# Optimization experiments

Hardware: AMD Instinct MI355X
Metric: run time of the kernel (lower is better)

The kernel has to match this reference:

```python
import jax, jax.numpy as jnp
import numpy as np
from jax import lax

N_NODES = 5000; N_EDGES = 160000; N_FEAT = 128; HIDDEN = 256
N_TPL = 10; N_TPL_NODES = 10; N_CLASSES = 8
ALPHA = 0.5          # FGW structure/feature trade-off
CG_ITERS = 5         # conditional-gradient (Frank-Wolfe) outer iterations
SINK_ITERS = 30      # log-domain Sinkhorn iterations (EMD surrogate)
SINK_REG = 0.02      # entropic reg relative to cost scale


def setup_inputs() -> dict:
    key = jax.random.key(0)
    ks = jax.random.split(key, 8)
    x = jax.random.normal(ks[0], (N_NODES, N_FEAT), jnp.float32)
    edge_index = jax.random.randint(ks[1], (2, N_EDGES), 0, N_NODES)
    W1 = jax.random.normal(ks[2], (N_FEAT, HIDDEN), jnp.float32) / np.sqrt(N_FEAT)
    b1 = jnp.zeros((HIDDEN,), jnp.float32)
    W2 = jax.random.normal(ks[3], (HIDDEN, N_FEAT), jnp.float32) / np.sqrt(HIDDEN)
    b2 = jnp.zeros((N_FEAT,), jnp.float32)
    templates = jax.random.uniform(ks[4], (N_TPL, N_TPL_NODES, N_TPL_NODES), jnp.float32)
    templates_features = jax.random.uniform(ks[5], (N_TPL, N_TPL_NODES, N_FEAT), jnp.float32)
    Wlin = jax.random.normal(ks[6], (N_TPL, N_CLASSES), jnp.float32) / np.sqrt(N_TPL)
    blin = jnp.zeros((N_CLASSES,), jnp.float32)
    return dict(x=x, edge_index=edge_index, W1=W1, b1=b1, W2=W2, b2=b2,
                templates=templates, templates_features=templates_features,
                Wlin=Wlin, blin=blin)


def gcn_conv(x, src, dst, W, b):
    # PyG GCNConv: x @ W, then D^-1/2 (A + I) D^-1/2 aggregation, then + b
    n = x.shape[0]
    loop = jnp.arange(n)
    s = jnp.concatenate([src, loop]); d = jnp.concatenate([dst, loop])
    deg = jax.ops.segment_sum(jnp.ones(s.shape[0], x.dtype), d, num_segments=n)
    dinv = lax.rsqrt(jnp.maximum(deg, 1.0))
    h = x @ W
    msg = h[s] * (dinv[s] * dinv[d])[:, None]
    return jax.ops.segment_sum(msg, d, num_segments=n) + b


def sinkhorn_log(G, logp, logq):
    # entropic OT in log domain as a jit-friendly surrogate for exact EMD
    scale = lax.stop_gradient(jnp.max(jnp.abs(G)) + 1e-9)
    mlogK = -G / (SINK_REG * scale)          # [n, m]
    f0 = jnp.zeros(G.shape[0], G.dtype); g0 = jnp.zeros(G.shape[1], G.dtype)
    def body(carry, _):
        f, g = carry
        g = logq - jax.nn.logsumexp(mlogK + f[:, None], axis=0)
        f = logp - jax.nn.logsumexp(mlogK + g[None, :], axis=1)
        return (f, g), None
    (f, g), _ = lax.scan(body, (f0, g0), None, length=SINK_ITERS)
    return jnp.exp(f[:, None] + mlogK + g[None, :])


def fgw2(C1, x, C2, F2):
    # Fused Gromov-Wasserstein distance (square loss), uniform weights,
    # conditional-gradient with fixed step 2/(t+2) and Sinkhorn LP surrogate.
    n, m = C1.shape[0], C2.shape[0]
    p = jnp.full((n,), 1.0 / n, x.dtype); q = jnp.full((m,), 1.0 / m, x.dtype)
    logp = jnp.log(p); logq = jnp.log(q)
    # squared-euclidean feature cost  [n, m]
    M = jnp.sum(x * x, 1)[:, None] + jnp.sum(F2 * F2, 1)[None, :] - 2.0 * x @ F2.T
    # square-loss GW decomposition: f1=a^2, f2=b^2, h1=a, h2=2b
    constC = ((C1 * C1) @ p)[:, None] + ((C2 * C2) @ q)[None, :]
    def tens(T):
        return constC - C1 @ T @ (2.0 * C2).T
    T = p[:, None] * q[None, :]
    for t in range(CG_ITERS):
        grad = (1.0 - ALPHA) * M + 2.0 * ALPHA * tens(T)
        Tnew = sinkhorn_log(grad, logp, logq)
        T = T + (2.0 / (t + 2.0)) * (Tnew - T)
    return (1.0 - ALPHA) * jnp.sum(M * T) + ALPHA * jnp.sum(tens(T) * T)


def reference(x, edge_index, W1, b1, W2, b2, templates, templates_features, Wlin, blin):
    src, dst = edge_index[0], edge_index[1]
    h = jax.nn.relu(gcn_conv(x, src, dst, W1, b1))
    h = gcn_conv(h, src, dst, W2, b2)           # [N, F]
    n = x.shape[0]
    C = jnp.zeros((n, n), x.dtype).at[src, dst].set(1.0)   # dense adjacency
    dists = jax.vmap(lambda Ct, Ft: fgw2(C, h, Ct, Ft))(templates, templates_features)  # [K]
    return dists @ Wlin + blin                  # [num_classes]
```

## Files before the change

kernel.cpp:

```cpp
#include <hip/hip_runtime.h>
#include <cstdint>

#define NND 5000
#define NE 160000
#define NF 128
#define NH 256
#define NT 10
#define MT 10
#define NC 8
#define NMAT (NND*MT)
#define CG_ITERS 5
#define SINK_IT 30

#if __has_builtin(__builtin_amdgcn_update_dpp)
#define DPP_ADD(x, ctrl, rmask) \
    ((x) + __int_as_float(__builtin_amdgcn_update_dpp(0, __float_as_int(x), (ctrl), (rmask), 0xf, true)))
__device__ __forceinline__ float wave_sum63(float x) {
    x = DPP_ADD(x, 0x111, 0xf);
    x = DPP_ADD(x, 0x112, 0xf);
    x = DPP_ADD(x, 0x114, 0xf);
    x = DPP_ADD(x, 0x118, 0xf);
    x = DPP_ADD(x, 0x142, 0xa);
    x = DPP_ADD(x, 0x143, 0xc);
    return x;
}
#else
__device__ __forceinline__ float wave_sum63(float x) {
#pragma unroll
    for (int off = 32; off; off >>= 1) x += __shfl_xor(x, off);
    return x;
}
#endif

__device__ __forceinline__ float frcp(float x) {
#if __has_builtin(__builtin_amdgcn_rcpf)
    return __builtin_amdgcn_rcpf(x);
#else
    return 1.f / x;
#endif
}


__global__ void k_edge1(const int* __restrict__ src, const int* __restrict__ dst,
                        int* __restrict__ cntD, unsigned* __restrict__ bitmap,
                        int* __restrict__ cntS, unsigned char* __restrict__ keep) {
    for (int e = blockIdx.x*blockDim.x + threadIdx.x; e < NE; e += gridDim.x*blockDim.x) {
        int s = src[e], d = dst[e];
        atomicAdd(&cntD[d], 1);
        int key = s * NND + d;
        unsigned bit = 1u << (key & 31);
        unsigned old = atomicOr(&bitmap[key >> 5], bit);
        if (!(old & bit)) { keep[e] = 1; atomicAdd(&cntS[s], 1); }
        else keep[e] = 0;
    }
}

__global__ void k_exscan2(const int* __restrict__ cntD, int* __restrict__ rpD,
                          float* __restrict__ dinv,
                          const int* __restrict__ cntS, int* __restrict__ rpS,
                          float* __restrict__ c1row,
                          const float* __restrict__ tpl, float* __restrict__ c2row) {
    const int T = 1024;
    int tid = threadIdx.x;
    if (blockIdx.x == 2) {
        if (tid < NT * MT) {
            int t = tid / MT, j = tid % MT;
            float s = 0.f;
            for (int k = 0; k < MT; k++) { float v = tpl[t * 100 + j * 10 + k]; s += v * v; }
            c2row[tid] = s * (1.f / MT);
        }
        return;
    }
    const int* cnt = blockIdx.x ? cntS : cntD;
    int* rp = blockIdx.x ? rpS : rpD;
    int C = (NND + T - 1) / T;
    int begin = tid * C, end = begin + C; if (end > NND) end = NND; if (begin > NND) begin = NND;
    int s = 0;
    for (int i = begin; i < end; i++) s += cnt[i];
    __shared__ int part[1024];
    part[tid] = s; __syncthreads();
    for (int off = 1; off < T; off <<= 1) {
        int v = (tid >= off) ? part[tid - off] : 0;
        __syncthreads();
        part[tid] += v;
        __syncthreads();
    }
    int run = part[tid] - s;
    for (int i = begin; i < end; i++) { rp[i] = run; run += cnt[i]; }
    if (tid == T - 1) rp[NND] = part[T - 1];
    if (blockIdx.x == 0)
        for (int i = begin; i < end; i++) dinv[i] = rsqrtf((float)(cnt[i] + 1));
    else
        for (int i = begin; i < end; i++) c1row[i] = (float)cnt[i] * (1.f / NND);
}

__global__ void k_scatter2(const int* __restrict__ src, const int* __restrict__ dst,
                           const unsigned char* __restrict__ keep,
                           const int* __restrict__ rpD, int* __restrict__ cur1,
                           int* __restrict__ csrS, float* __restrict__ csrC,
                           const float* __restrict__ dinv,
                           const int* __restrict__ rpS, int* __restrict__ cur2,
                           int* __restrict__ csrD) {
    for (int e = blockIdx.x*blockDim.x + threadIdx.x; e < NE; e += gridDim.x*blockDim.x) {
        int s = src[e], d = dst[e];
        int pos = rpD[d] + atomicAdd(&cur1[d], 1);
        csrS[pos] = s;
        csrC[pos] = dinv[s] * dinv[d];
        if (keep[e]) {
            int p2 = rpS[s] + atomicAdd(&cur2[s], 1);
            csrD[p2] = d;
        }
    }
}


__global__ __launch_bounds__(256) void k_gemm(const float* __restrict__ A,
                                              const float* __restrict__ B,
                                              float* __restrict__ C, int M, int N, int K,
                                              const float* __restrict__ bias, int relu) {
    const int BM = 64, BN = 64, BK = 16;
    __shared__ float As[BK][BM + 1];
    __shared__ float Bs[BK][BN];
    int tid = threadIdx.x;
    int row0 = blockIdx.y * BM, col0 = blockIdx.x * BN;
    int tx = tid % 16, ty = tid / 16;
    float acc[4][4] = {};
    for (int k0 = 0; k0 < K; k0 += BK) {
#pragma unroll
        for (int l = 0; l < 4; l++) {
            int idx = tid + l * 256;
            int r = idx / BK, kk = idx % BK;
            int gr = row0 + r;
            As[kk][r] = (gr < M) ? A[(size_t)gr * K + k0 + kk] : 0.f;
        }
#pragma unroll
        for (int l = 0; l < 4; l++) {
            int idx = tid + l * 256;
            int kk = idx / BN, c = idx % BN;
            Bs[kk][c] = B[(size_t)(k0 + kk) * N + col0 + c];
        }
        __syncthreads();
#pragma unroll
        for (int kk = 0; kk < BK; kk++) {
            float a[4], b[4];
#pragma unroll
            for (int i = 0; i < 4; i++) a[i] = As[kk][ty * 4 + i];
#pragma unroll
            for (int j = 0; j < 4; j++) b[j] = Bs[kk][tx * 4 + j];
#pragma unroll
            for (int i = 0; i < 4; i++)
#pragma unroll
                for (int j = 0; j < 4; j++) acc[i][j] += a[i] * b[j];
        }
        __syncthreads();
    }
#pragma unroll
    for (int i = 0; i < 4; i++) {
        int gr = row0 + ty * 4 + i;
        if (gr < M) {
#pragma unroll
            for (int j = 0; j < 4; j++) {
                int gc = col0 + tx * 4 + j;
                float o = acc[i][j];
                if (bias) o += bias[gc];
                if (relu) o = fmaxf(o, 0.f);
                C[(size_t)gr * N + gc] = o;
            }
        }
    }
}

__global__ __launch_bounds__(256) void k_aggregate(const float4* __restrict__ hin4,
                            const float* __restrict__ bias,
                            float4* __restrict__ hout4, const int* __restrict__ rp,
                            const int* __restrict__ csrS, const float* __restrict__ csrC,
                            const float* __restrict__ dinv) {
    int v = blockIdx.x * 8 + (threadIdx.x >> 5);
    int l = threadIdx.x & 31;
    float dv = dinv[v];
    float sc = dv * dv;
    float4 a = hin4[(size_t)v * 32 + l];
    float4 acc = make_float4(a.x * sc, a.y * sc, a.z * sc, a.w * sc);
    int e0 = rp[v], e1 = rp[v + 1];
    for (int e = e0; e < e1; e++) {
        int s = csrS[e];
        float c = csrC[e];
        float4 hv = hin4[(size_t)s * 32 + l];
        acc.x = fmaf(hv.x, c, acc.x);
        acc.y = fmaf(hv.y, c, acc.y);
        acc.z = fmaf(hv.z, c, acc.z);
        acc.w = fmaf(hv.w, c, acc.w);
    }
    if (bias) {
        float4 bb = ((const float4*)bias)[l];
        acc.x += bb.x; acc.y += bb.y; acc.z += bb.z; acc.w += bb.w;
    }
    hout4[(size_t)v * 32 + l] = acc;
}


__global__ __launch_bounds__(128) void k_M(const float* __restrict__ h,
                    const float* __restrict__ tplF,
                    float* __restrict__ Mout, float* __restrict__ T) {
    int i = blockIdx.x;
    int tid = threadIdx.x;
    int lane = tid & 63, w = tid >> 6;
    __shared__ float hrow[NF];
    __shared__ float part[2];
    float hv = h[(size_t)i * NF + tid];
    hrow[tid] = hv;
    float ps = wave_sum63(hv * hv);
    if (lane == 63) part[w] = ps;
    __syncthreads();
    float sx = part[0] + part[1];
    int c = tid;
    if (c < NT * MT) {
        const float4* Fc = (const float4*)(tplF + (size_t)c * NF);
        const float4* hr = (const float4*)hrow;
        float dot = 0.f, nrm = 0.f;
#pragma unroll 8
        for (int f = 0; f < NF / 4; f++) {
            float4 fv = Fc[f];
            float4 hq = hr[f];
            dot = fmaf(hq.x, fv.x, dot); dot = fmaf(hq.y, fv.y, dot);
            dot = fmaf(hq.z, fv.z, dot); dot = fmaf(hq.w, fv.w, dot);
            nrm = fmaf(fv.x, fv.x, nrm); nrm = fmaf(fv.y, fv.y, nrm);
            nrm = fmaf(fv.z, fv.z, nrm); nrm = fmaf(fv.w, fv.w, nrm);
        }
        int t = c / MT, j = c % MT;
        Mout[(size_t)t * NMAT + (size_t)i * MT + j] = sx + nrm - 2.f * dot;
        T[(size_t)t * NMAT + (size_t)i * MT + j] = 1.f / (float)NMAT;
    }
}


__global__ __launch_bounds__(256) void k_grad(const float* __restrict__ T, const float* __restrict__ Mm,
                                              const float* __restrict__ c1row, const float* __restrict__ c2row,
                                              const float* __restrict__ tpl,
                                              const int* __restrict__ rpS, const int* __restrict__ csrD,
                                              float* __restrict__ G, unsigned* __restrict__ scaleBits) {
    int t = blockIdx.y;
    int tid = threadIdx.x;
    __shared__ float tC2[100];
    if (tid < 100) tC2[tid] = 2.f * tpl[t * 100 + tid];
    __syncthreads();
    int i = blockIdx.x * 256 + tid;
    float amax = 0.f;
    if (i < NND) {
        const float* Tt = T + (size_t)t * NMAT;
        const float* Mt = Mm + (size_t)t * NMAT;
        float* Gt = G + (size_t)t * NMAT;
        float L[MT];
#pragma unroll
        for (int j = 0; j < MT; j++) L[j] = 0.f;
        int e0 = rpS[i], e1 = rpS[i + 1];
        for (int e = e0; e < e1; e++) {
            int k = csrD[e];
            const float* Tk = Tt + (size_t)k * MT;
#pragma unroll
            for (int j = 0; j < MT; j++) L[j] += Tk[j];
        }
        float c1 = c1row[i];
#pragma unroll
        for (int j = 0; j < MT; j++) {
            float s = 0.f;
#pragma unroll
            for (int k = 0; k < MT; k++) s += L[k] * tC2[j * 10 + k];
            float g = 0.5f * Mt[(size_t)i * MT + j] + (c1 + c2row[t * 10 + j] - s);
            Gt[(size_t)i * MT + j] = g;
            amax = fmaxf(amax, fabsf(g));
        }
    }
    __shared__ float red[256];
    red[tid] = amax; __syncthreads();
    for (int off = 128; off > 0; off >>= 1) {
        if (tid < off) red[tid] = fmaxf(red[tid], red[tid + off]);
        __syncthreads();
    }
    if (tid == 0) atomicMax(&scaleBits[t], __float_as_uint(red[0]));
}

__global__ __attribute__((amdgpu_flat_work_group_size(512, 512), amdgpu_waves_per_eu(2, 2)))
void k_sinkhorn(const float* __restrict__ G,
                const unsigned* __restrict__ scaleBits,
                float* __restrict__ T, float step) {
    int t = blockIdx.x;
    int tid = threadIdx.x;
    int lane = tid & 63, w = tid >> 6;
    float sc = __uint_as_float(scaleBits[t]) + 1e-9f;
    float inv = -1.f / (0.02f * sc);
    const float* Gt = G + (size_t)t * NMAT;
    float* Tt = T + (size_t)t * NMAT;

    __shared__ float wred[8][10];
    __shared__ float4 vbc4[3];

    float Kf[10][10];
    float u[10];
#pragma unroll
    for (int r = 0; r < 10; r++) {
        int i = tid + r * 512;
        if (i < NND) {
            u[r] = 1.f;
            const float2* Gr = (const float2*)(Gt + (size_t)i * 10);
#pragma unroll
            for (int h = 0; h < 5; h++) {
                float2 g = Gr[h];
                Kf[r][2*h]   = __expf(g.x * inv);
                Kf[r][2*h+1] = __expf(g.y * inv);
            }
        } else {
            u[r] = 0.f;
#pragma unroll
            for (int j = 0; j < 10; j++) Kf[r][j] = 0.f;
        }
    }

    float vv[10];

    for (int it = 0; it < SINK_IT; it++) {
        float S[10];
#pragma unroll
        for (int j = 0; j < 10; j++) S[j] = 0.f;
#pragma unroll
        for (int r = 0; r < 10; r++) {
            float ur = u[r];
#pragma unroll
            for (int j = 0; j < 10; j++) S[j] = fmaf(Kf[r][j], ur, S[j]);
        }
#pragma unroll
        for (int j = 0; j < 10; j++) {
            float s = wave_sum63(S[j]);
            if (lane == 63) wred[w][j] = s;
        }
        __syncthreads();
        if (tid < 10) {
            float s = 0.f;
#pragma unroll
            for (int q = 0; q < 8; q++) s += wred[q][tid];
            ((float*)vbc4)[tid] = 0.1f * frcp(fmaxf(s, 1e-30f));
        }
        __syncthreads();
        {
            float4 a = vbc4[0], b = vbc4[1], c = vbc4[2];
            vv[0]=a.x; vv[1]=a.y; vv[2]=a.z; vv[3]=a.w;
            vv[4]=b.x; vv[5]=b.y; vv[6]=b.z; vv[7]=b.w;
            vv[8]=c.x; vv[9]=c.y;
        }
#pragma unroll
        for (int r = 0; r < 10; r++) {
            float R = 0.f;
#pragma unroll
            for (int j = 0; j < 10; j++) R = fmaf(Kf[r][j], vv[j], R);
            u[r] = (tid + r * 512 < NND) ? (2e-4f * frcp(fmaxf(R, 1e-30f))) : 0.f;
        }
    }

#pragma unroll
    for (int r = 0; r < 10; r++) {
        int i = tid + r * 512;
        if (i < NND) {
            float ur = u[r];
            float2* Tr = (float2*)(Tt + (size_t)i * 10);
#pragma unroll
            for (int h = 0; h < 5; h++) {
                float2 v = Tr[h];
                v.x += step * (ur * Kf[r][2*h]   * vv[2*h]   - v.x);
                v.y += step * (ur * Kf[r][2*h+1] * vv[2*h+1] - v.y);
                Tr[h] = v;
            }
        }
    }
}


__global__ __launch_bounds__(256) void k_final(const float* __restrict__ T, const float* __restrict__ Mm,
                                               const float* __restrict__ c1row, const float* __restrict__ c2row,
                                               const float* __restrict__ tpl,
                                               const int* __restrict__ rpS, const int* __restrict__ csrD,
                                               double* __restrict__ dd, int* __restrict__ done,
                                               const float* __restrict__ Wlin,
                                               const float* __restrict__ blin,
                                               float* __restrict__ out) {
    int t = blockIdx.y;
    int tid = threadIdx.x;
    __shared__ float tC2[100];
    if (tid < 100) tC2[tid] = 2.f * tpl[t * 100 + tid];
    __syncthreads();
    int i = blockIdx.x * 256 + tid;
    double msum = 0.0, tsum = 0.0;
    if (i < NND) {
        const float* Tt = T + (size_t)t * NMAT;
        const float* Mt = Mm + (size_t)t * NMAT;
        float L[MT];
#pragma unroll
        for (int j = 0; j < MT; j++) L[j] = 0.f;
        int e0 = rpS[i], e1 = rpS[i + 1];
        for (int e = e0; e < e1; e++) {
            int k = csrD[e];
            const float* Tk = Tt + (size_t)k * MT;
#pragma unroll
            for (int j = 0; j < MT; j++) L[j] += Tk[j];
        }
        float c1 = c1row[i];
#pragma unroll
        for (int j = 0; j < MT; j++) {
            float s = 0.f;
#pragma unroll
            for (int k = 0; k < MT; k++) s += L[k] * tC2[j * 10 + k];
            float ts = c1 + c2row[t * 10 + j] - s;
            float Tv = Tt[(size_t)i * MT + j];
            msum += (double)(Mt[(size_t)i * MT + j] * Tv);
            tsum += (double)(ts * Tv);
        }
    }
    __shared__ double r1[256], r2[256];
    r1[tid] = msum; r2[tid] = tsum; __syncthreads();
    for (int off = 128; off > 0; off >>= 1) {
        if (tid < off) { r1[tid] += r1[tid + off]; r2[tid] += r2[tid + off]; }
        __syncthreads();
    }
    if (tid == 0) {
        atomicAdd(&dd[t * 2], r1[0]);
        atomicAdd(&dd[t * 2 + 1], r2[0]);
        __threadfence();
        int prev = atomicAdd(done, 1);
        if (prev == 20 * NT - 1) {
            __threadfence();
            float ds[NT];
#pragma unroll
            for (int k = 0; k < NT; k++) {
                unsigned long long b0 = __hip_atomic_load((unsigned long long*)&dd[2*k],
                                        __ATOMIC_RELAXED, __HIP_MEMORY_SCOPE_AGENT);
                unsigned long long b1 = __hip_atomic_load((unsigned long long*)&dd[2*k+1],
                                        __ATOMIC_RELAXED, __HIP_MEMORY_SCOPE_AGENT);
                ds[k] = 0.5f * (float)(__longlong_as_double(b0) + __longlong_as_double(b1));
            }
#pragma unroll
            for (int c = 0; c < NC; c++) {
                float o = blin[c];
#pragma unroll
                for (int k = 0; k < NT; k++) o = fmaf(ds[k], Wlin[k * NC + c], o);
                out[c] = o;
            }
        }
    }
}


extern "C" void kernel_launch(void* const* d_in, const int* in_sizes, int n_in,
                              void* d_out, int out_size, void* d_ws, size_t ws_size,
                              hipStream_t stream) {
    const float* x    = (const float*)d_in[0];
    const int*   ei   = (const int*)d_in[1];
    const int*   src  = ei;
    const int*   dst  = ei + NE;
    const float* W1   = (const float*)d_in[2];
    const float* b1   = (const float*)d_in[3];
    const float* W2   = (const float*)d_in[4];
    const float* b2   = (const float*)d_in[5];
    const float* tpl  = (const float*)d_in[6];
    const float* tplF = (const float*)d_in[7];
    const float* Wlin = (const float*)d_in[8];
    const float* blin = (const float*)d_in[9];
    float* out = (float*)d_out;

    char* w = (char*)d_ws;
    size_t off = 0;
    auto alloc = [&](size_t b) -> char* {
        off = (off + 255) & ~(size_t)255;
        char* p = w + off; off += b; return p;
    };
    float* bufA = (float*)alloc((size_t)NND * NH * 4);
    float* bufB = (float*)alloc((size_t)NND * NH * 4);
    float* bufH = (float*)alloc((size_t)NND * NF * 4);
    float* Mm   = (float*)alloc((size_t)NT * NMAT * 4);
    float* T    = (float*)alloc((size_t)NT * NMAT * 4);
    float* G    = (float*)alloc((size_t)NT * NMAT * 4);
    int* cntD = (int*)alloc((size_t)NND * 4);
    int* cntS = (int*)alloc((size_t)NND * 4);
    int* cur1 = (int*)alloc((size_t)NND * 4);
    int* cur2 = (int*)alloc((size_t)NND * 4);
    double* dd = (double*)alloc((size_t)NT * 2 * 8);
    int* done = (int*)alloc(4);
    unsigned* scaleArr = (unsigned*)alloc((size_t)CG_ITERS * NT * 4);
    char* zend = w + off;
    unsigned* bitmap = (unsigned*)alloc((size_t)781250 * 4);
    int* rpD  = (int*)alloc((size_t)(NND + 1) * 4);
    int* rpS  = (int*)alloc((size_t)(NND + 1) * 4);
    int* csrS = (int*)alloc((size_t)NE * 4);
    float* csrC = (float*)alloc((size_t)NE * 4);
    int* csrD2 = (int*)alloc((size_t)NE * 4);
    unsigned char* keep = (unsigned char*)alloc((size_t)NE);
    float* dinv  = (float*)alloc((size_t)NND * 4);
    float* c1row = (float*)alloc((size_t)NND * 4);
    float* c2row = (float*)alloc((size_t)100 * 4);

    hipMemsetAsync(cntD, 0, (size_t)(zend - (char*)cntD), stream);
    hipMemsetAsync(bitmap, 0, (size_t)781250 * 4, stream);

    k_edge1<<<625, 256, 0, stream>>>(src, dst, cntD, bitmap, cntS, keep);
    k_exscan2<<<3, 1024, 0, stream>>>(cntD, rpD, dinv, cntS, rpS, c1row, tpl, c2row);
    k_scatter2<<<625, 256, 0, stream>>>(src, dst, keep, rpD, cur1, csrS, csrC, dinv,
                                        rpS, cur2, csrD2);

    k_aggregate<<<625, 256, 0, stream>>>((const float4*)x, nullptr, (float4*)bufA,
                                         rpD, csrS, csrC, dinv);
    k_gemm<<<dim3(NH / 64, (NND + 63) / 64), 256, 0, stream>>>(bufA, W1, bufB, NND, NH, NF, b1, 1);
    k_gemm<<<dim3(NF / 64, (NND + 63) / 64), 256, 0, stream>>>(bufB, W2, bufA, NND, NF, NH, nullptr, 0);
    k_aggregate<<<625, 256, 0, stream>>>((const float4*)bufA, b2, (float4*)bufH,
                                         rpD, csrS, csrC, dinv);

    k_M<<<NND, 128, 0, stream>>>(bufH, tplF, Mm, T);

    for (int t = 0; t < CG_ITERS; t++) {
        unsigned* sb = scaleArr + t * NT;
        k_grad<<<dim3(20, NT), 256, 0, stream>>>(T, Mm, c1row, c2row, tpl, rpS, csrD2, G, sb);
        float step = 2.f / (float)(t + 2);
        k_sinkhorn<<<NT, 512, 0, stream>>>(G, sb, T, step);
    }

    k_final<<<dim3(20, NT), 256, 0, stream>>>(T, Mm, c1row, c2row, tpl, rpS, csrD2,
                                              dd, done, Wlin, blin, out);
}
```

Baseline: 687.7 us.

## Fuse second aggregation with cost build, pad rows, skip first gradient kernel

The second GCN aggregation is merged into the cost-matrix kernel. That kernel also computes the first CG gradient in closed form, using the fact that T starts uniform, plus per-row maxima, so the first k_grad launch is dropped. Transport-plan, cost and gradient rows are padded to 12 floats to allow float4/float2 vector loads. Other changes: the bitmap is cleared by the single shared memset, the GEMM shared-memory padding is adjusted, and one bounds check is dropped in Sinkhorn. The fused kernel now does per-feature scalar gathers instead of float4, and memory use grows.

```diff
diff --git a/kernel.cpp b/kernel.cpp
--- a/kernel.cpp
+++ b/kernel.cpp
@@ -9,12 +9,16 @@
 #define MT 10
 #define NC 8
 #define NMAT (NND*MT)
+#define ROWP 12
+#define NMATP (NND*ROWP)
 #define CG_ITERS 5
 #define SINK_IT 30
 
 #if __has_builtin(__builtin_amdgcn_update_dpp)
 #define DPP_ADD(x, ctrl, rmask) \
     ((x) + __int_as_float(__builtin_amdgcn_update_dpp(0, __float_as_int(x), (ctrl), (rmask), 0xf, true)))
+#define DPP_MAX(x, ctrl, rmask) \
+    fmaxf((x), __int_as_float(__builtin_amdgcn_update_dpp(0, __float_as_int(x), (ctrl), (rmask), 0xf, true)))
 __device__ __forceinline__ float wave_sum63(float x) {
     x = DPP_ADD(x, 0x111, 0xf);
     x = DPP_ADD(x, 0x112, 0xf);
@@ -24,10 +28,24 @@
     x = DPP_ADD(x, 0x143, 0xc);
     return x;
 }
+__device__ __forceinline__ float wave_max63(float x) {
+    x = DPP_MAX(x, 0x111, 0xf);
+    x = DPP_MAX(x, 0x112, 0xf);
+    x = DPP_MAX(x, 0x114, 0xf);
+    x = DPP_MAX(x, 0x118, 0xf);
+    x = DPP_MAX(x, 0x142, 0xa);
+    x = DPP_MAX(x, 0x143, 0xc);
+    return x;
+}
 #else
 __device__ __forceinline__ float wave_sum63(float x) {
 #pragma unroll
     for (int off = 32; off; off >>= 1) x += __shfl_xor(x, off);
+    return x;
+}
+__device__ __forceinline__ float wave_max63(float x) {
+#pragma unroll
+    for (int off = 32; off; off >>= 1) x = fmaxf(x, __shfl_xor(x, off));
     return x;
 }
 #endif
@@ -59,15 +77,20 @@
                           float* __restrict__ dinv,
                           const int* __restrict__ cntS, int* __restrict__ rpS,
                           float* __restrict__ c1row,
-                          const float* __restrict__ tpl, float* __restrict__ c2row) {
+                          const float* __restrict__ tpl, float* __restrict__ c2row,
+                          float* __restrict__ rsT) {
     const int T = 1024;
     int tid = threadIdx.x;
     if (blockIdx.x == 2) {
         if (tid < NT * MT) {
             int t = tid / MT, j = tid % MT;
-            float s = 0.f;
-            for (int k = 0; k < MT; k++) { float v = tpl[t * 100 + j * 10 + k]; s += v * v; }
+            float s = 0.f, rs = 0.f;
+            for (int k = 0; k < MT; k++) {
+                float v = tpl[t * 100 + j * 10 + k];
+                s += v * v; rs += v;
+            }
             c2row[tid] = s * (1.f / MT);
+            rsT[tid] = rs;
         }
         return;
     }
@@ -119,7 +142,7 @@
                                               float* __restrict__ C, int M, int N, int K,
                                               const float* __restrict__ bias, int relu) {
     const int BM = 64, BN = 64, BK = 16;
-    __shared__ float As[BK][BM + 1];
+    __shared__ float As[BK][BM + 4];
     __shared__ float Bs[BK][BN];
     int tid = threadIdx.x;
     int row0 = blockIdx.y * BM, col0 = blockIdx.x * BN;
@@ -171,7 +194,6 @@
 }
 
 __global__ __launch_bounds__(256) void k_aggregate(const float4* __restrict__ hin4,
-                            const float* __restrict__ bias,
                             float4* __restrict__ hout4, const int* __restrict__ rp,
                             const int* __restrict__ csrS, const float* __restrict__ csrC,
                             const float* __restrict__ dinv) {
@@ -191,25 +213,32 @@
         acc.z = fmaf(hv.z, c, acc.z);
         acc.w = fmaf(hv.w, c, acc.w);
     }
-    if (bias) {
-        float4 bb = ((const float4*)bias)[l];
-        acc.x += bb.x; acc.y += bb.y; acc.z += bb.z; acc.w += bb.w;
-    }
     hout4[(size_t)v * 32 + l] = acc;
 }
 
-
-__global__ __launch_bounds__(128) void k_M(const float* __restrict__ h,
+__global__ __launch_bounds__(128) void k_fuse(const float* __restrict__ t2,
+                    const float* __restrict__ b2,
+                    const int* __restrict__ rp, const int* __restrict__ csrS,
+                    const float* __restrict__ csrC, const float* __restrict__ dinv,
                     const float* __restrict__ tplF,
-                    float* __restrict__ Mout, float* __restrict__ T) {
+                    const float* __restrict__ c1row, const int* __restrict__ cntS,
+                    const float* __restrict__ c2row, const float* __restrict__ rsT,
+                    float* __restrict__ Mm, float* __restrict__ G,
+                    float* __restrict__ T, float* __restrict__ pmax) {
     int i = blockIdx.x;
     int tid = threadIdx.x;
     int lane = tid & 63, w = tid >> 6;
     __shared__ float hrow[NF];
     __shared__ float part[2];
-    float hv = h[(size_t)i * NF + tid];
-    hrow[tid] = hv;
-    float ps = wave_sum63(hv * hv);
+    __shared__ float sMax[112];
+    float dv = dinv[i];
+    float acc = t2[(size_t)i * NF + tid] * (dv * dv);
+    int e0 = rp[i], e1 = rp[i + 1];
+    for (int e = e0; e < e1; e++)
+        acc = fmaf(t2[(size_t)csrS[e] * NF + tid], csrC[e], acc);
+    acc += b2[tid];
+    hrow[tid] = acc;
+    float ps = wave_sum63(acc * acc);
     if (lane == 63) part[w] = ps;
     __syncthreads();
     float sx = part[0] + part[1];
@@ -227,9 +256,22 @@
             nrm = fmaf(fv.x, fv.x, nrm); nrm = fmaf(fv.y, fv.y, nrm);
             nrm = fmaf(fv.z, fv.z, nrm); nrm = fmaf(fv.w, fv.w, nrm);
         }
+        float m = sx + nrm - 2.f * dot;
         int t = c / MT, j = c % MT;
-        Mout[(size_t)t * NMAT + (size_t)i * MT + j] = sx + nrm - 2.f * dot;
-        T[(size_t)t * NMAT + (size_t)i * MT + j] = 1.f / (float)NMAT;
+        size_t base = (size_t)t * NMATP + (size_t)i * ROWP + j;
+        Mm[base] = m;
+        T[base] = 1.f / (float)NMAT;
+        float g = 0.5f * m + c1row[i] + c2row[c]
+                - ((float)cntS[i] * (1.f / NMAT)) * (2.f * rsT[c]);
+        G[base] = g;
+        sMax[c] = fabsf(g);
+    }
+    __syncthreads();
+    if (tid < NT) {
+        float m = sMax[tid * 10];
+#pragma unroll
+        for (int k = 1; k < 10; k++) m = fmaxf(m, sMax[tid * 10 + k]);
+        pmax[(size_t)tid * NND + i] = m;
     }
 }
 
@@ -247,29 +289,39 @@
     int i = blockIdx.x * 256 + tid;
     float amax = 0.f;
     if (i < NND) {
-        const float* Tt = T + (size_t)t * NMAT;
-        const float* Mt = Mm + (size_t)t * NMAT;
-        float* Gt = G + (size_t)t * NMAT;
-        float L[MT];
-#pragma unroll
-        for (int j = 0; j < MT; j++) L[j] = 0.f;
+        const float* Tt = T + (size_t)t * NMATP;
+        float4 A0 = make_float4(0.f,0.f,0.f,0.f);
+        float4 A1 = make_float4(0.f,0.f,0.f,0.f);
+        float2 A2 = make_float2(0.f,0.f);
         int e0 = rpS[i], e1 = rpS[i + 1];
         for (int e = e0; e < e1; e++) {
             int k = csrD[e];
-            const float* Tk = Tt + (size_t)k * MT;
-#pragma unroll
-            for (int j = 0; j < MT; j++) L[j] += Tk[j];
-        }
+            const float4* Tk = (const float4*)(Tt + (size_t)k * ROWP);
+            float4 x0 = Tk[0], x1 = Tk[1];
+            float2 x2 = ((const float2*)Tk)[4];
+            A0.x += x0.x; A0.y += x0.y; A0.z += x0.z; A0.w += x0.w;
+            A1.x += x1.x; A1.y += x1.y; A1.z += x1.z; A1.w += x1.w;
+            A2.x += x2.x; A2.y += x2.y;
+        }
+        float L[10] = {A0.x, A0.y, A0.z, A0.w, A1.x, A1.y, A1.z, A1.w, A2.x, A2.y};
+        const float4* Mt4 = (const float4*)(Mm + (size_t)t * NMATP + (size_t)i * ROWP);
+        float4 m0 = Mt4[0], m1 = Mt4[1];
+        float2 m2 = ((const float2*)Mt4)[4];
+        float m[10] = {m0.x, m0.y, m0.z, m0.w, m1.x, m1.y, m1.z, m1.w, m2.x, m2.y};
         float c1 = c1row[i];
+        float g[10];
 #pragma unroll
         for (int j = 0; j < MT; j++) {
             float s = 0.f;
 #pragma unroll
-            for (int k = 0; k < MT; k++) s += L[k] * tC2[j * 10 + k];
-            float g = 0.5f * Mt[(size_t)i * MT + j] + (c1 + c2row[t * 10 + j] - s);
-            Gt[(size_t)i * MT + j] = g;
-            amax = fmaxf(amax, fabsf(g));
-        }
+            for (int k = 0; k < MT; k++) s = fmaf(L[k], tC2[j * 10 + k], s);
+            g[j] = 0.5f * m[j] + (c1 + c2row[t * 10 + j] - s);
+            amax = fmaxf(amax, fabsf(g[j]));
+        }
+        float4* Gt4 = (float4*)(G + (size_t)t * NMATP + (size_t)i * ROWP);
+        Gt4[0] = make_float4(g[0], g[1], g[2], g[3]);
+        Gt4[1] = make_float4(g[4], g[5], g[6], g[7]);
+        ((float2*)Gt4)[4] = make_float2(g[8], g[9]);
     }
     __shared__ float red[256];
     red[tid] = amax; __syncthreads();
@@ -283,17 +335,38 @@
 __global__ __attribute__((amdgpu_flat_work_group_size(512, 512), amdgpu_waves_per_eu(2, 2)))
 void k_sinkhorn(const float* __restrict__ G,
                 const unsigned* __restrict__ scaleBits,
+                const float* __restrict__ pmax,
                 float* __restrict__ T, float step) {
     int t = blockIdx.x;
     int tid = threadIdx.x;
     int lane = tid & 63, w = tid >> 6;
-    float sc = __uint_as_float(scaleBits[t]) + 1e-9f;
-    float inv = -1.f / (0.02f * sc);
-    const float* Gt = G + (size_t)t * NMAT;
-    float* Tt = T + (size_t)t * NMAT;
 
     __shared__ float wred[8][10];
     __shared__ float4 vbc4[3];
+    __shared__ float scsh;
+
+    float sc;
+    if (pmax) {
+        const float* pm = pmax + (size_t)t * NND;
+        float m = 0.f;
+        for (int k = tid; k < NND; k += 512) m = fmaxf(m, pm[k]);
+        m = wave_max63(m);
+        if (lane == 63) wred[w][0] = m;
+        __syncthreads();
+        if (tid == 0) {
+            float mm = wred[0][0];
+#pragma unroll
+            for (int q = 1; q < 8; q++) mm = fmaxf(mm, wred[q][0]);
+            scsh = mm;
+        }
+        __syncthreads();
+        sc = scsh;
+    } else {
+        sc = __uint_as_float(scaleBits[t]);
+    }
+    float inv = -1.f / (0.02f * (sc + 1e-9f));
+    const float* Gt = G + (size_t)t * NMATP;
+    float* Tt = T + (size_t)t * NMATP;
 
     float Kf[10][10];
     float u[10];
@@ -302,13 +375,14 @@
         int i = tid + r * 512;
         if (i < NND) {
             u[r] = 1.f;
-            const float2* Gr = (const float2*)(Gt + (size_t)i * 10);
-#pragma unroll
-            for (int h = 0; h < 5; h++) {
-                float2 g = Gr[h];
-                Kf[r][2*h]   = __expf(g.x * inv);
-                Kf[r][2*h+1] = __expf(g.y * inv);
-            }
+            const float4* Gr = (const float4*)(Gt + (size_t)i * ROWP);
+            float4 ga = Gr[0], gb = Gr[1];
+            float2 gc = ((const float2*)Gr)[4];
+            Kf[r][0] = __expf(ga.x * inv); Kf[r][1] = __expf(ga.y * inv);
+            Kf[r][2] = __expf(ga.z * inv); Kf[r][3] = __expf(ga.w * inv);
+            Kf[r][4] = __expf(gb.x * inv); Kf[r][5] = __expf(gb.y * inv);
+            Kf[r][6] = __expf(gb.z * inv); Kf[r][7] = __expf(gb.w * inv);
+            Kf[r][8] = __expf(gc.x * inv); Kf[r][9] = __expf(gc.y * inv);
         } else {
             u[r] = 0.f;
 #pragma unroll
@@ -352,7 +426,7 @@
             float R = 0.f;
 #pragma unroll
             for (int j = 0; j < 10; j++) R = fmaf(Kf[r][j], vv[j], R);
-            u[r] = (tid + r * 512 < NND) ? (2e-4f * frcp(fmaxf(R, 1e-30f))) : 0.f;
+            u[r] = 2e-4f * frcp(fmaxf(R, 1e-30f));
         }
     }
 
@@ -361,14 +435,21 @@
         int i = tid + r * 512;
         if (i < NND) {
             float ur = u[r];
-            float2* Tr = (float2*)(Tt + (size_t)i * 10);
-#pragma unroll
-            for (int h = 0; h < 5; h++) {
-                float2 v = Tr[h];
-                v.x += step * (ur * Kf[r][2*h]   * vv[2*h]   - v.x);
-                v.y += step * (ur * Kf[r][2*h+1] * vv[2*h+1] - v.y);
-                Tr[h] = v;
-            }
+            float4* Tr4 = (float4*)(Tt + (size_t)i * ROWP);
+            float4 t0 = Tr4[0], t1 = Tr4[1];
+            float2 t2v = ((float2*)Tr4)[4];
+            t0.x += step * (ur * Kf[r][0] * vv[0] - t0.x);
+            t0.y += step * (ur * Kf[r][1] * vv[1] - t0.y);
+            t0.z += step * (ur * Kf[r][2] * vv[2] - t0.z);
+            t0.w += step * (ur * Kf[r][3] * vv[3] - t0.w);
+            t1.x += step * (ur * Kf[r][4] * vv[4] - t1.x);
+            t1.y += step * (ur * Kf[r][5] * vv[5] - t1.y);
+            t1.z += step * (ur * Kf[r][6] * vv[6] - t1.z);
+            t1.w += step * (ur * Kf[r][7] * vv[7] - t1.w);
+            t2v.x += step * (ur * Kf[r][8] * vv[8] - t2v.x);
+            t2v.y += step * (ur * Kf[r][9] * vv[9] - t2v.y);
+            Tr4[0] = t0; Tr4[1] = t1;
+            ((float2*)Tr4)[4] = t2v;
         }
     }
 }
@@ -390,28 +471,38 @@
     int i = blockIdx.x * 256 + tid;
     double msum = 0.0, tsum = 0.0;
     if (i < NND) {
-        const float* Tt = T + (size_t)t * NMAT;
-        const float* Mt = Mm + (size_t)t * NMAT;
-        float L[MT];
-#pragma unroll
-        for (int j = 0; j < MT; j++) L[j] = 0.f;
+        const float* Tt = T + (size_t)t * NMATP;
+        float4 A0 = make_float4(0.f,0.f,0.f,0.f);
+        float4 A1 = make_float4(0.f,0.f,0.f,0.f);
+        float2 A2 = make_float2(0.f,0.f);
         int e0 = rpS[i], e1 = rpS[i + 1];
         for (int e = e0; e < e1; e++) {
             int k = csrD[e];
-            const float* Tk = Tt + (size_t)k * MT;
-#pragma unroll
-            for (int j = 0; j < MT; j++) L[j] += Tk[j];
-        }
+            const float4* Tk = (const float4*)(Tt + (size_t)k * ROWP);
+            float4 x0 = Tk[0], x1 = Tk[1];
+            float2 x2 = ((const float2*)Tk)[4];
+            A0.x += x0.x; A0.y += x0.y; A0.z += x0.z; A0.w += x0.w;
+            A1.x += x1.x; A1.y += x1.y; A1.z += x1.z; A1.w += x1.w;
+            A2.x += x2.x; A2.y += x2.y;
+        }
+        float L[10] = {A0.x, A0.y, A0.z, A0.w, A1.x, A1.y, A1.z, A1.w, A2.x, A2.y};
+        const float4* Mt4 = (const float4*)(Mm + (size_t)t * NMATP + (size_t)i * ROWP);
+        float4 m0 = Mt4[0], m1 = Mt4[1];
+        float2 m2 = ((const float2*)Mt4)[4];
+        float m[10] = {m0.x, m0.y, m0.z, m0.w, m1.x, m1.y, m1.z, m1.w, m2.x, m2.y};
+        const float4* Ti4 = (const float4*)(Tt + (size_t)i * ROWP);
+        float4 tv0 = Ti4[0], tv1 = Ti4[1];
+        float2 tv2 = ((const float2*)Ti4)[4];
+        float Tv[10] = {tv0.x, tv0.y, tv0.z, tv0.w, tv1.x, tv1.y, tv1.z, tv1.w, tv2.x, tv2.y};
         float c1 = c1row[i];
 #pragma unroll
         for (int j = 0; j < MT; j++) {
             float s = 0.f;
 #pragma unroll
-            for (int k = 0; k < MT; k++) s += L[k] * tC2[j * 10 + k];
+            for (int k = 0; k < MT; k++) s = fmaf(L[k], tC2[j * 10 + k], s);
             float ts = c1 + c2row[t * 10 + j] - s;
-            float Tv = Tt[(size_t)i * MT + j];
-            msum += (double)(Mt[(size_t)i * MT + j] * Tv);
-            tsum += (double)(ts * Tv);
+            msum += (double)(m[j] * Tv[j]);
+            tsum += (double)(ts * Tv[j]);
         }
     }
     __shared__ double r1[256], r2[256];
@@ -473,10 +564,10 @@
     };
     float* bufA = (float*)alloc((size_t)NND * NH * 4);
     float* bufB = (float*)alloc((size_t)NND * NH * 4);
-    float* bufH = (float*)alloc((size_t)NND * NF * 4);
-    float* Mm   = (float*)alloc((size_t)NT * NMAT * 4);
-    float* T    = (float*)alloc((size_t)NT * NMAT * 4);
-    float* G    = (float*)alloc((size_t)NT * NMAT * 4);
+    float* Mm   = (float*)alloc((size_t)NT * NMATP * 4);
+    float* T    = (float*)alloc((size_t)NT * NMATP * 4);
+    float* G    = (float*)alloc((size_t)NT * NMATP * 4);
+    float* pmax = (float*)alloc((size_t)NT * NND * 4);
     int* cntD = (int*)alloc((size_t)NND * 4);
     int* cntS = (int*)alloc((size_t)NND * 4);
     int* cur1 = (int*)alloc((size_t)NND * 4);
@@ -484,8 +575,8 @@
     double* dd = (double*)alloc((size_t)NT * 2 * 8);
     int* done = (int*)alloc(4);
     unsigned* scaleArr = (unsigned*)alloc((size_t)CG_ITERS * NT * 4);
+    unsigned* bitmap = (unsigned*)alloc((size_t)781250 * 4);
     char* zend = w + off;
-    unsigned* bitmap = (unsigned*)alloc((size_t)781250 * 4);
     int* rpD  = (int*)alloc((size_t)(NND + 1) * 4);
     int* rpS  = (int*)alloc((size_t)(NND + 1) * 4);
     int* csrS = (int*)alloc((size_t)NE * 4);
@@ -495,29 +586,29 @@
     float* dinv  = (float*)alloc((size_t)NND * 4);
     float* c1row = (float*)alloc((size_t)NND * 4);
     float* c2row = (float*)alloc((size_t)100 * 4);
+    float* rsT   = (float*)alloc((size_t)100 * 4);
 
     hipMemsetAsync(cntD, 0, (size_t)(zend - (char*)cntD), stream);
-    hipMemsetAsync(bitmap, 0, (size_t)781250 * 4, stream);
 
     k_edge1<<<625, 256, 0, stream>>>(src, dst, cntD, bitmap, cntS, keep);
-    k_exscan2<<<3, 1024, 0, stream>>>(cntD, rpD, dinv, cntS, rpS, c1row, tpl, c2row);
+    k_exscan2<<<3, 1024, 0, stream>>>(cntD, rpD, dinv, cntS, rpS, c1row, tpl, c2row, rsT);
     k_scatter2<<<625, 256, 0, stream>>>(src, dst, keep, rpD, cur1, csrS, csrC, dinv,
                                         rpS, cur2, csrD2);
 
-    k_aggregate<<<625, 256, 0, stream>>>((const float4*)x, nullptr, (float4*)bufA,
+    k_aggregate<<<625, 256, 0, stream>>>((const float4*)x, (float4*)bufA,
                                          rpD, csrS, csrC, dinv);
     k_gemm<<<dim3(NH / 64, (NND + 63) / 64), 256, 0, stream>>>(bufA, W1, bufB, NND, NH, NF, b1, 1);
     k_gemm<<<dim3(NF / 64, (NND + 63) / 64), 256, 0, stream>>>(bufB, W2, bufA, NND, NF, NH, nullptr, 0);
-    k_aggregate<<<625, 256, 0, stream>>>((const float4*)bufA, b2, (float4*)bufH,
-                                         rpD, csrS, csrC, dinv);
-
-    k_M<<<NND, 128, 0, stream>>>(bufH, tplF, Mm, T);
+
+    k_fuse<<<NND, 128, 0, stream>>>(bufA, b2, rpD, csrS, csrC, dinv, tplF,
+                                    c1row, cntS, c2row, rsT, Mm, G, T, pmax);
 
     for (int t = 0; t < CG_ITERS; t++) {
         unsigned* sb = scaleArr + t * NT;
-        k_grad<<<dim3(20, NT), 256, 0, stream>>>(T, Mm, c1row, c2row, tpl, rpS, csrD2, G, sb);
+        if (t > 0)
+            k_grad<<<dim3(20, NT), 256, 0, stream>>>(T, Mm, c1row, c2row, tpl, rpS, csrD2, G, sb);
         float step = 2.f / (float)(t + 2);
-        k_sinkhorn<<<NT, 512, 0, stream>>>(G, sb, T, step);
+        k_sinkhorn<<<NT, 512, 0, stream>>>(G, sb, (t == 0) ? pmax : nullptr, T, step);
     }
 
     k_final<<<dim3(20, NT), 256, 0, stream>>>(T, Mm, c1row, c2row, tpl, rpS, csrD2,
```

Measured after the change: 658.8 us. 1.04x faster.
